# Optimization experiments

Measured on AMD Instinct MI355X. Metric: run time of the kernel, lower is better.

The kernel has to match this reference:

```python
import jax, jax.numpy as jnp
import numpy as np

N_DIS = 5000
N_GEN = 20000
N = N_DIS + N_GEN
E = 400000
N_MIRNA = 2000
EMB = 128
HID = 64


def setup_inputs() -> dict:
    key = jax.random.key(0)
    ks = jax.random.split(key, 20)
    def g(k, shape, scale=0.05):
        return jax.random.normal(k, shape, dtype=jnp.float32) * scale
    return {
        'd_features': g(ks[0], (N_DIS, 383), 1.0),
        'g_features': g(ks[1], (N_GEN, 4395), 1.0),
        'miRNA_dis': jax.random.uniform(ks[2], (N_MIRNA, N_DIS), dtype=jnp.float32),
        'gene_dis': jax.random.uniform(ks[3], (N_GEN, N_DIS), dtype=jnp.float32),
        'Wd': g(ks[4], (383, EMB)),
        'bd': jnp.zeros((EMB,), jnp.float32),
        'Wg': g(ks[5], (4395, EMB)),
        'bg': jnp.zeros((EMB,), jnp.float32),
        'W1': g(ks[6], (N_MIRNA, EMB)),
        'W4': g(ks[7], (N_DIS, EMB)),
        'Ws1': g(ks[8], (EMB, HID)),
        'Wn1': g(ks[9], (EMB, HID)),
        'b1': jnp.zeros((HID,), jnp.float32),
        'Ws2': g(ks[10], (HID, HID)),
        'Wn2': g(ks[11], (HID, HID)),
        'b2': jnp.zeros((HID,), jnp.float32),
        'src': jax.random.randint(ks[12], (E,), 0, N, dtype=jnp.int32),
        'dst': jax.random.randint(ks[13], (E,), 0, N, dtype=jnp.int32),
    }


def _sage_mean(h, src, dst, Ws, Wn, b):
    # DGL SAGEConv 'mean': fc_self(h) + fc_neigh(mean over in-neighbors) + bias
    msg = h[src]                                            # [E, d] gather
    agg = jax.ops.segment_sum(msg, dst, num_segments=N)     # [N, d] scatter-add
    deg = jax.ops.segment_sum(jnp.ones((dst.shape[0],), h.dtype), dst, num_segments=N)
    neigh = agg / jnp.maximum(deg, 1.0)[:, None]            # mean (zero-deg -> 0)
    return h @ Ws + neigh @ Wn + b


def reference(d_features, g_features, miRNA_dis, gene_dis, Wd, bd, Wg, bg,
              W1, W4, Ws1, Wn1, b1, Ws2, Wn2, b2, src, dst):
    # CrossCompressUnit outputs used by forward: A2 = M1^T W1, B1 = M2 W4
    A2 = miRNA_dis.T @ W1          # [N_DIS, EMB]
    B1 = gene_dis @ W4             # [N_GEN, EMB]
    # Node embeddings (dropout is identity at inference; torch.no_grad block)
    h_dis = 0.9 * (d_features @ Wd + bd) + 0.1 * A2   # [N_DIS, EMB]
    h_gen = 0.9 * (g_features @ Wg + bg) + 0.1 * B1   # [N_GEN, EMB]
    h = jnp.concatenate([h_dis, h_gen], axis=0)        # [N, EMB]
    h = _sage_mean(h, src, dst, Ws1, Wn1, b1)          # [N, 64]
    h = jax.nn.relu(h)
    h = _sage_mean(h, src, dst, Ws2, Wn2, b2)          # [N, 64]
    return h
```

## Files before the change

kernel.cpp:

```cpp
#include <hip/hip_runtime.h>

#define NDIS 5000
#define NGEN 20000
#define NTOT 25000
#define EDG  400000

typedef __attribute__((ext_vector_type(8))) short short8;
typedef __attribute__((ext_vector_type(4))) float f32x4;
typedef __attribute__((ext_vector_type(4), aligned(4))) float f32x4u;
typedef __attribute__((ext_vector_type(4))) unsigned int uint4v;
typedef __attribute__((ext_vector_type(2))) unsigned int uint2v;
typedef __attribute__((ext_vector_type(2), aligned(4))) unsigned int uint2a;

constexpr size_t AL(size_t x) { return (x + 255) & ~(size_t)255; }
constexpr size_t OFF_H0   = 0;
constexpr size_t OFF_PQ   = AL(OFF_H0  + (size_t)NTOT * 128 * 4);
constexpr size_t OFF_H1   = AL(OFF_PQ  + (size_t)NTOT * 128 * 4);
constexpr size_t OFF_DEG  = AL(OFF_H1  + (size_t)NTOT * 128 * 4);
constexpr size_t OFF_RS   = AL(OFF_DEG + (size_t)NTOT * 4);
constexpr size_t OFF_CUR  = AL(OFF_RS  + (size_t)(NTOT + 1) * 4);
constexpr size_t OFF_ESRC = AL(OFF_CUR + (size_t)NTOT * 4);
constexpr size_t OFF_MIT  = AL(OFF_ESRC + (size_t)EDG * 4);
constexpr size_t OFF_BDIS = AL(OFF_MIT + (size_t)5000 * 2048 * 2);
constexpr size_t OFF_BGEN = AL(OFF_BDIS + (size_t)8 * 76 * 512 * 2);
constexpr size_t OFF_BS1  = AL(OFF_BGEN + (size_t)8 * 300 * 512 * 2);
constexpr size_t OFF_BS2  = AL(OFF_BS1 + (size_t)8 * 4 * 512 * 2);

__device__ __forceinline__ ushort f2bf(float f) {
    unsigned u = __float_as_uint(f);
    u += 0x7fffu + ((u >> 16) & 1u);
    return (ushort)(u >> 16);
}

__device__ __forceinline__ unsigned cvtpk(float a, float b) {
    unsigned r;
    asm("v_cvt_pk_bf16_f32 %0, %1, %2" : "=v"(r) : "v"(a), "v"(b));
    return r;
}

__device__ __forceinline__ void MFMA(f32x4& d, short8 a, short8 b) {
    asm volatile("v_mfma_f32_16x16x32_bf16 %0, %1, %2, %0"
                 : "+v"(d) : "v"(a), "v"(b));
}

struct TcvtIns { const float* p[9]; };

__global__ __launch_bounds__(256) void k_tcvt_multi(TcvtIns ins, char* ws)
{
    constexpr int   TR[9]   = {383, 2000, 4395, 5000, 2000, 128, 128, 64, 64};
    constexpr int   TC[9]   = {128, 128, 128, 128, 5000, 64, 64, 64, 64};
    constexpr int   TKT[9]  = {76, 76, 300, 300, 2048 , 4, 4, 4, 4};
    constexpr int   TKO[9]  = {0, 12, 0, 140, 0, 0, 0, 0, 0};
    constexpr int   TRP[9]  = {384, 2048, 4480, 5120, 2048, 128, 128, 128, 128};
    constexpr int   TNOFF[9]= {0, 0, 0, 0, 0, 0, 64, 0, 64};
    constexpr int   TMODE[9]= {1, 1, 1, 1, 0, 1, 1, 1, 1};
    constexpr float TSC[9]  = {0.9f, 0.1f, 0.9f, 0.1f, 1.f, 1.f, 1.f, 1.f, 1.f};
    constexpr size_t TOUT[9]= {OFF_BDIS, OFF_BDIS, OFF_BGEN, OFF_BGEN, OFF_MIT,
                               OFF_BS1, OFF_BS1, OFF_BS2, OFF_BS2};
    constexpr int TNBX[9]   = {4, 4, 4, 4, 157, 2, 2, 2, 2};
    constexpr int PRE[10]   = {0, 48, 304, 864, 1504, 11552, 11560, 11568, 11576, 11584};

    int bid = blockIdx.x;
    int d = 0;
#pragma unroll
    for (int q = 1; q < 9; ++q) if (bid >= PRE[q]) d = q;
    int local = bid - PRE[d];
    int bx = local % TNBX[d], by = local / TNBX[d];
    const int R = TR[d], C = TC[d], KT = TKT[d], KO = TKO[d];
    const int Rp = TRP[d], noff = TNOFF[d];
    const float scale = TSC[d];
    const float* in = ins.p[d];
    ushort* out = (ushort*)(ws + TOUT[d]);

    __shared__ float t[32][33];
    int tx = threadIdx.x & 31, ty = threadIdx.x >> 5;
    int c0 = bx * 32, r0 = by * 32;
#pragma unroll
    for (int j = 0; j < 4; ++j) {
        int r = r0 + ty + j * 8, c = c0 + tx;
        t[ty + j * 8][tx] = (r < R && c < C) ? in[(size_t)r * C + c] : 0.f;
    }
    __syncthreads();
#pragma unroll
    for (int j = 0; j < 4; ++j) {
        int c = c0 + ty + j * 8, r = r0 + tx;
        if (c >= C || r >= Rp) continue;
        ushort bv = f2bf(scale * t[tx][ty + j * 8]);
        if (TMODE[d] == 0) {
            out[(size_t)c * KT + r] = bv;
        } else {
            int n = noff + c, k = r;
            out[(size_t)((n >> 4) * KT + KO + (k >> 5)) * 512 +
                ((k >> 3) & 3) * 128 + (n & 15) * 8 + (k & 7)] = bv;
        }
    }
}

template<int A2MODE, bool ATOMIC>
__global__ __launch_bounds__(256, 2) void gemm_st(
    const float* __restrict__ A1, int lda1, long lim1, int nst1,
    const void* __restrict__ A2v, int lda2, long lim2, int nst2,
    const ushort* __restrict__ Bf, int KT,
    float* __restrict__ C, int M, const float* __restrict__ bias)
{
    __shared__ ushort ldsH0[64 * 128];
    __shared__ ushort ldsL0[64 * 128];
    __shared__ ushort ldsH1[64 * 128];
    __shared__ ushort ldsL1[64 * 128];
    const int tid  = threadIdx.x;
    const int lane = tid & 63;
    const int w    = tid >> 6;
    const int fr = lane & 15, kq = lane >> 4;
    const int bm0 = blockIdx.x * 64;

    const int NSTT = nst1 + nst2;
    const int per = (NSTT + gridDim.y - 1) / gridDim.y;
    const int s0 = blockIdx.y * per;
    const int s1 = min(NSTT, s0 + per);
    const int NT = s1 - s0;
    if (NT <= 0) return;

    f32x4 acc[4][2];
#pragma unroll
    for (int i = 0; i < 4; ++i) { acc[i][0] = {0.f,0.f,0.f,0.f}; acc[i][1] = {0.f,0.f,0.f,0.f}; }

    uint4v faA[8], faB[8];
    short8 Breg0[4][2], Breg1[4][2];

    const int srow = w * 16 + (lane >> 5);
    const int scol = lane & 31;

    auto issueA = [&](int stg, uint4v* fa) {
        const bool r1 = (A2MODE == 0) || (stg < nst1);
#pragma unroll
        for (int i = 0; i < 8; ++i) {
            int r = bm0 + srow + i * 2;
            if (r1) {
                long e = (long)r * lda1 + (long)(stg << 7) + scol * 4;
                if (e > lim1 - 4) e = lim1 - 4;
                fa[i] = __builtin_bit_cast(uint4v, *(const f32x4u*)(A1 + e));
            } else if (A2MODE == 1) {
                long e = (long)r * lda2 + (long)((stg - nst1) << 7) + scol * 4;
                if (e > lim2 - 4) e = lim2 - 4;
                fa[i] = __builtin_bit_cast(uint4v, *(const f32x4u*)((const float*)A2v + e));
            } else {
                long e = (long)r * lda2 + (long)((stg - nst1) << 7) + scol * 4;
                if (e > lim2 - 4) e = lim2 - 4;
                uint2a v = *(const uint2a*)((const ushort*)A2v + e);
                fa[i][0] = v[0]; fa[i][1] = v[1];
            }
        }
    };
    auto issueB = [&](int stg, short8 (*BR)[2]) {
#pragma unroll
        for (int ks = 0; ks < 4; ++ks)
#pragma unroll
            for (int nf = 0; nf < 2; ++nf)
                BR[ks][nf] = *(const short8*)(
                    Bf + (size_t)((w * 2 + nf) * KT + stg * 4 + ks) * 512 + lane * 8);
    };
    auto writeT = [&](int stg, const uint4v* fa, ushort* bufH, ushort* bufL) {
        const bool cvt = (A2MODE != 2) || (stg < nst1);
        const int G = scol >> 1, h = lane & 1;
#pragma unroll
        for (int i = 0; i < 8; ++i) {
            int r = srow + i * 2;
            const size_t off = (size_t)r * 256 + ((G ^ (r & 7)) << 4) + h * 8;
            uint2v dh, dl;
            if (cvt) {
                f32x4 v = __builtin_bit_cast(f32x4, fa[i]);
                dh[0] = cvtpk(v[0], v[1]);
                dh[1] = cvtpk(v[2], v[3]);
                float h0f = __uint_as_float(dh[0] << 16);
                float h1f = __uint_as_float(dh[0] & 0xffff0000u);
                float h2f = __uint_as_float(dh[1] << 16);
                float h3f = __uint_as_float(dh[1] & 0xffff0000u);
                dl[0] = cvtpk(v[0] - h0f, v[1] - h1f);
                dl[1] = cvtpk(v[2] - h2f, v[3] - h3f);
            } else {
                dh[0] = fa[i][0]; dh[1] = fa[i][1];
                dl[0] = 0u; dl[1] = 0u;
            }
            *(uint2v*)((char*)bufH + off) = dh;
            *(uint2v*)((char*)bufL + off) = dl;
        }
    };

#define PHASE(T, BR, LDSH, LDSL, FAW, LWH, LWL)                              \
    {                                                                        \
        const int x7 = fr & 7;                                               \
        _Pragma("unroll")                                                    \
        for (int ks = 0; ks < 4; ++ks) {                                     \
            short8 af[4], al[4];                                             \
            _Pragma("unroll")                                                \
            for (int mf = 0; mf < 4; ++mf) {                                 \
                const int so = (((ks * 4 + kq) ^ x7) << 3);                  \
                af[mf] = *(const short8*)&LDSH[fr * 128 + mf * 2048 + so];   \
                al[mf] = *(const short8*)&LDSL[fr * 128 + mf * 2048 + so];   \
            }                                                                \
            _Pragma("unroll")                                                \
            for (int mf = 0; mf < 4; ++mf) {                                 \
                MFMA(acc[mf][0], af[mf], BR[ks][0]);                         \
                MFMA(acc[mf][1], af[mf], BR[ks][1]);                         \
                MFMA(acc[mf][0], al[mf], BR[ks][0]);                         \
                MFMA(acc[mf][1], al[mf], BR[ks][1]);                         \
            }                                                                \
        }                                                                    \
        if ((T) + 2 < NT) issueB(s0 + (T) + 2, BR);                          \
        __builtin_amdgcn_s_barrier();                                        \
        if ((T) + 1 < NT) {                                                  \
            writeT(s0 + (T) + 1, FAW, LWH, LWL);                             \
            if ((T) + 3 < NT) issueA(s0 + (T) + 3, FAW);                     \
            asm volatile("s_waitcnt lgkmcnt(0)" ::: "memory");               \
            __builtin_amdgcn_s_barrier();                                    \
        }                                                                    \
    }

    issueA(s0, faA); issueB(s0, Breg0);
    if (NT > 1) { issueA(s0 + 1, faB); issueB(s0 + 1, Breg1); }
    writeT(s0, faA, ldsH0, ldsL0);
    if (NT > 2) issueA(s0 + 2, faA);
    asm volatile("s_waitcnt lgkmcnt(0)" ::: "memory");
    __builtin_amdgcn_s_barrier();

    for (int t = 0; t < NT; t += 2) {
        PHASE(t, Breg0, ldsH0, ldsL0, faB, ldsH1, ldsL1);
        if (t + 1 < NT) PHASE(t + 1, Breg1, ldsH1, ldsL1, faA, ldsH0, ldsL0);
    }
#undef PHASE

    asm volatile("s_nop 7\n\ts_nop 7\n\ts_nop 7" ::: "memory");
#pragma unroll
    for (int mf = 0; mf < 4; ++mf)
#pragma unroll
        for (int nf = 0; nf < 2; ++nf)
#pragma unroll
            for (int r = 0; r < 4; ++r) {
                int row = bm0 + mf * 16 + kq * 4 + r;
                if (row < M) {
                    int col = w * 32 + nf * 16 + fr;
                    if (ATOMIC) {
                        atomicAdd(&C[(size_t)row * 128 + col], acc[mf][nf][r]);
                    } else {
                        float v = acc[mf][nf][r];
                        if (col < 64) v += bias[col];
                        C[(size_t)row * 128 + col] = v;
                    }
                }
            }
}

__global__ void k_binit(float* __restrict__ h0, const float* __restrict__ bd,
                        const float* __restrict__ bg) {
    int i = blockIdx.x * 256 + threadIdx.x;
    if (i >= NTOT * 128) return;
    int col = i & 127;
    h0[i] = 0.9f * ((i >> 7) < NDIS ? bd[col] : bg[col]);
}

__global__ void k_deg(const int* __restrict__ dst, int* __restrict__ deg, int E) {
    int e = blockIdx.x * blockDim.x + threadIdx.x;
    if (e < E) atomicAdd(&deg[dst[e]], 1);
}

__global__ __launch_bounds__(1024) void k_scan(const int* __restrict__ deg,
                                               int* __restrict__ row_start,
                                               int* __restrict__ cursor, int n) {
    __shared__ int wsum[16];
    __shared__ int carry_s;
    int t = threadIdx.x;
    int lane = t & 63, wid = t >> 6;
    if (t == 0) { carry_s = 0; row_start[0] = 0; }
    __syncthreads();
    for (int base = 0; base < n; base += 1024) {
        int i = base + t;
        int v = (i < n) ? deg[i] : 0;
        int x = v;
#pragma unroll
        for (int off = 1; off < 64; off <<= 1) {
            int y = __shfl_up(x, off, 64);
            if (lane >= off) x += y;
        }
        if (lane == 63) wsum[wid] = x;
        __syncthreads();
        if (wid == 0) {
            int s = (lane < 16) ? wsum[lane] : 0;
#pragma unroll
            for (int off = 1; off < 16; off <<= 1) {
                int y = __shfl_up(s, off, 64);
                if (lane >= off) s += y;
            }
            if (lane < 16) wsum[lane] = s;
        }
        __syncthreads();
        int pre = (wid > 0 ? wsum[wid - 1] : 0) + carry_s;
        int incl = x + pre;
        if (i < n) { row_start[i + 1] = incl; cursor[i] = incl - v; }
        __syncthreads();
        if (t == 1023) carry_s = incl;
        __syncthreads();
    }
}

__global__ void k_fill(const int* __restrict__ src, const int* __restrict__ dst,
                       int* __restrict__ cursor, int* __restrict__ esrc, int E) {
    int e = blockIdx.x * blockDim.x + threadIdx.x;
    if (e < E) {
        int pos = atomicAdd(&cursor[dst[e]], 1);
        esrc[pos] = src[e];
    }
}

__global__ __launch_bounds__(64) void k_agg(const float* __restrict__ PQ,
                                            const int* __restrict__ rs,
                                            const int* __restrict__ esrc,
                                            float* __restrict__ out, int ldout, int relu)
{
    int n = blockIdx.x, t = threadIdx.x;
    int s0 = rs[n], s1 = rs[n + 1];
    float a0 = 0.f, a1 = 0.f, a2 = 0.f, a3 = 0.f;
    int i = s0;
    for (; i + 4 <= s1; i += 4) {
        int e0 = esrc[i], e1 = esrc[i + 1], e2 = esrc[i + 2], e3 = esrc[i + 3];
        a0 += PQ[(size_t)e0 * 128 + 64 + t];
        a1 += PQ[(size_t)e1 * 128 + 64 + t];
        a2 += PQ[(size_t)e2 * 128 + 64 + t];
        a3 += PQ[(size_t)e3 * 128 + 64 + t];
    }
    for (; i < s1; ++i) a0 += PQ[(size_t)esrc[i] * 128 + 64 + t];
    float s = (a0 + a1) + (a2 + a3);
    float dg = (float)(s1 - s0);
    s /= fmaxf(dg, 1.f);
    float v = PQ[(size_t)n * 128 + t] + s;
    if (relu) v = fmaxf(v, 0.f);
    out[(size_t)n * ldout + t] = v;
}

extern "C" void kernel_launch(void* const* d_in, const int* in_sizes, int n_in,
                              void* d_out, int out_size, void* d_ws, size_t ws_size,
                              hipStream_t stream)
{
    const float* d_features = (const float*)d_in[0];
    const float* g_features = (const float*)d_in[1];
    const float* miRNA_dis  = (const float*)d_in[2];
    const float* gene_dis   = (const float*)d_in[3];
    const float* Wd  = (const float*)d_in[4];
    const float* bd  = (const float*)d_in[5];
    const float* Wg  = (const float*)d_in[6];
    const float* bg  = (const float*)d_in[7];
    const float* W1  = (const float*)d_in[8];
    const float* W4  = (const float*)d_in[9];
    const float* Ws1 = (const float*)d_in[10];
    const float* Wn1 = (const float*)d_in[11];
    const float* b1  = (const float*)d_in[12];
    const float* Ws2 = (const float*)d_in[13];
    const float* Wn2 = (const float*)d_in[14];
    const float* b2  = (const float*)d_in[15];
    const int* src = (const int*)d_in[16];
    const int* dst = (const int*)d_in[17];
    (void)in_sizes; (void)n_in; (void)out_size; (void)ws_size;

    char* ws = (char*)d_ws;
    float*  h0   = (float*)(ws + OFF_H0);
    float*  PQ   = (float*)(ws + OFF_PQ);
    float*  h1   = (float*)(ws + OFF_H1);
    int*    deg  = (int*)(ws + OFF_DEG);
    int*    rs   = (int*)(ws + OFF_RS);
    int*    cur  = (int*)(ws + OFF_CUR);
    int*    esrc = (int*)(ws + OFF_ESRC);
    ushort* miT  = (ushort*)(ws + OFF_MIT);
    ushort* Bdis = (ushort*)(ws + OFF_BDIS);
    ushort* Bgen = (ushort*)(ws + OFF_BGEN);
    ushort* Bs1  = (ushort*)(ws + OFF_BS1);
    ushort* Bs2  = (ushort*)(ws + OFF_BS2);

    hipMemsetAsync(deg, 0, (size_t)NTOT * 4, stream);
    hipMemsetAsync(h1, 0, (size_t)NTOT * 128 * 4, stream);
    k_deg<<<(EDG + 255) / 256, 256, 0, stream>>>(dst, deg, EDG);
    k_scan<<<1, 1024, 0, stream>>>(deg, rs, cur, NTOT);
    k_fill<<<(EDG + 255) / 256, 256, 0, stream>>>(src, dst, cur, esrc, EDG);

    TcvtIns ins;
    ins.p[0] = Wd;  ins.p[1] = W1;  ins.p[2] = Wg;  ins.p[3] = W4;
    ins.p[4] = miRNA_dis; ins.p[5] = Ws1; ins.p[6] = Wn1; ins.p[7] = Ws2; ins.p[8] = Wn2;
    k_tcvt_multi<<<11584, 256, 0, stream>>>(ins, ws);

    k_binit<<<(NTOT * 128 + 255) / 256, 256, 0, stream>>>(h0, bd, bg);
    gemm_st<2, true><<<dim3(79, 5), 256, 0, stream>>>(
        d_features, 383, (long)NDIS * 383, 3,
        miT, 2048, (long)NDIS * 2048, 16, Bdis, 76, h0, NDIS, nullptr);
    gemm_st<1, true><<<dim3(313, 4), 256, 0, stream>>>(
        g_features, 4395, (long)NGEN * 4395, 35,
        gene_dis, 5000, (long)NGEN * 5000, 40, Bgen, 300,
        h0 + (size_t)NDIS * 128, NGEN, nullptr);

    gemm_st<0, false><<<dim3(391, 1), 256, 0, stream>>>(
        h0, 128, (long)NTOT * 128, 1, nullptr, 0, 0, 0, Bs1, 4, PQ, NTOT, b1);
    k_agg<<<NTOT, 64, 0, stream>>>(PQ, rs, esrc, h1, 128, 1);

    gemm_st<0, false><<<dim3(391, 1), 256, 0, stream>>>(
        h1, 128, (long)NTOT * 128, 1, nullptr, 0, 0, 0, Bs2, 4, PQ, NTOT, b2);
    k_agg<<<NTOT, 64, 0, stream>>>(PQ, rs, esrc, (float*)d_out, 64, 0);
}
```

Before: 376.3 us.

## Split concatenated-K embedding GEMMs into separate per-operand launches with own split-K

```diff
diff --git a/kernel.cpp b/kernel.cpp
--- a/kernel.cpp
+++ b/kernel.cpp
@@ -21,9 +21,11 @@
 constexpr size_t OFF_CUR  = AL(OFF_RS  + (size_t)(NTOT + 1) * 4);
 constexpr size_t OFF_ESRC = AL(OFF_CUR + (size_t)NTOT * 4);
 constexpr size_t OFF_MIT  = AL(OFF_ESRC + (size_t)EDG * 4);
-constexpr size_t OFF_BDIS = AL(OFF_MIT + (size_t)5000 * 2048 * 2);
-constexpr size_t OFF_BGEN = AL(OFF_BDIS + (size_t)8 * 76 * 512 * 2);
-constexpr size_t OFF_BS1  = AL(OFF_BGEN + (size_t)8 * 300 * 512 * 2);
+constexpr size_t OFF_BWD  = AL(OFF_MIT + (size_t)5000 * 2048 * 2);
+constexpr size_t OFF_BW1  = AL(OFF_BWD + (size_t)8 * 12 * 512 * 2);
+constexpr size_t OFF_BWG  = AL(OFF_BW1 + (size_t)8 * 64 * 512 * 2);
+constexpr size_t OFF_BW4  = AL(OFF_BWG + (size_t)8 * 140 * 512 * 2);
+constexpr size_t OFF_BS1  = AL(OFF_BW4 + (size_t)8 * 160 * 512 * 2);
 constexpr size_t OFF_BS2  = AL(OFF_BS1 + (size_t)8 * 4 * 512 * 2);
 
 __device__ __forceinline__ ushort f2bf(float f) {
@@ -49,13 +51,12 @@
 {
     constexpr int   TR[9]   = {383, 2000, 4395, 5000, 2000, 128, 128, 64, 64};
     constexpr int   TC[9]   = {128, 128, 128, 128, 5000, 64, 64, 64, 64};
-    constexpr int   TKT[9]  = {76, 76, 300, 300, 2048 , 4, 4, 4, 4};
-    constexpr int   TKO[9]  = {0, 12, 0, 140, 0, 0, 0, 0, 0};
+    constexpr int   TKT[9]  = {12, 64, 140, 160, 2048 , 4, 4, 4, 4};
     constexpr int   TRP[9]  = {384, 2048, 4480, 5120, 2048, 128, 128, 128, 128};
     constexpr int   TNOFF[9]= {0, 0, 0, 0, 0, 0, 64, 0, 64};
     constexpr int   TMODE[9]= {1, 1, 1, 1, 0, 1, 1, 1, 1};
     constexpr float TSC[9]  = {0.9f, 0.1f, 0.9f, 0.1f, 1.f, 1.f, 1.f, 1.f, 1.f};
-    constexpr size_t TOUT[9]= {OFF_BDIS, OFF_BDIS, OFF_BGEN, OFF_BGEN, OFF_MIT,
+    constexpr size_t TOUT[9]= {OFF_BWD, OFF_BW1, OFF_BWG, OFF_BW4, OFF_MIT,
                                OFF_BS1, OFF_BS1, OFF_BS2, OFF_BS2};
     constexpr int TNBX[9]   = {4, 4, 4, 4, 157, 2, 2, 2, 2};
     constexpr int PRE[10]   = {0, 48, 304, 864, 1504, 11552, 11560, 11568, 11576, 11584};
@@ -66,7 +67,7 @@
     for (int q = 1; q < 9; ++q) if (bid >= PRE[q]) d = q;
     int local = bid - PRE[d];
     int bx = local % TNBX[d], by = local / TNBX[d];
-    const int R = TR[d], C = TC[d], KT = TKT[d], KO = TKO[d];
+    const int R = TR[d], C = TC[d], KT = TKT[d];
     const int Rp = TRP[d], noff = TNOFF[d];
     const float scale = TSC[d];
     const float* in = ins.p[d];
@@ -90,7 +91,7 @@
             out[(size_t)c * KT + r] = bv;
         } else {
             int n = noff + c, k = r;
-            out[(size_t)((n >> 4) * KT + KO + (k >> 5)) * 512 +
+            out[(size_t)((n >> 4) * KT + (k >> 5)) * 512 +
                 ((k >> 3) & 3) * 128 + (n & 15) * 8 + (k & 7)] = bv;
         }
     }
@@ -139,10 +140,6 @@
                 long e = (long)r * lda1 + (long)(stg << 7) + scol * 4;
                 if (e > lim1 - 4) e = lim1 - 4;
                 fa[i] = __builtin_bit_cast(uint4v, *(const f32x4u*)(A1 + e));
-            } else if (A2MODE == 1) {
-                long e = (long)r * lda2 + (long)((stg - nst1) << 7) + scol * 4;
-                if (e > lim2 - 4) e = lim2 - 4;
-                fa[i] = __builtin_bit_cast(uint4v, *(const f32x4u*)((const float*)A2v + e));
             } else {
                 long e = (long)r * lda2 + (long)((stg - nst1) << 7) + scol * 4;
                 if (e > lim2 - 4) e = lim2 - 4;
@@ -369,8 +366,10 @@
     int*    cur  = (int*)(ws + OFF_CUR);
     int*    esrc = (int*)(ws + OFF_ESRC);
     ushort* miT  = (ushort*)(ws + OFF_MIT);
-    ushort* Bdis = (ushort*)(ws + OFF_BDIS);
-    ushort* Bgen = (ushort*)(ws + OFF_BGEN);
+    ushort* Bwd  = (ushort*)(ws + OFF_BWD);
+    ushort* Bw1  = (ushort*)(ws + OFF_BW1);
+    ushort* Bwg  = (ushort*)(ws + OFF_BWG);
+    ushort* Bw4  = (ushort*)(ws + OFF_BW4);
     ushort* Bs1  = (ushort*)(ws + OFF_BS1);
     ushort* Bs2  = (ushort*)(ws + OFF_BS2);
 
@@ -386,13 +385,18 @@
     k_tcvt_multi<<<11584, 256, 0, stream>>>(ins, ws);
 
     k_binit<<<(NTOT * 128 + 255) / 256, 256, 0, stream>>>(h0, bd, bg);
-    gemm_st<2, true><<<dim3(79, 5), 256, 0, stream>>>(
+    gemm_st<0, true><<<dim3(79, 1), 256, 0, stream>>>(
         d_features, 383, (long)NDIS * 383, 3,
-        miT, 2048, (long)NDIS * 2048, 16, Bdis, 76, h0, NDIS, nullptr);
-    gemm_st<1, true><<<dim3(313, 4), 256, 0, stream>>>(
+        nullptr, 0, 0, 0, Bwd, 12, h0, NDIS, nullptr);
+    gemm_st<2, true><<<dim3(79, 3), 256, 0, stream>>>(
+        nullptr, 0, 0, 0,
+        miT, 2048, (long)NDIS * 2048, 16, Bw1, 64, h0, NDIS, nullptr);
+    gemm_st<0, true><<<dim3(313, 6), 256, 0, stream>>>(
         g_features, 4395, (long)NGEN * 4395, 35,
-        gene_dis, 5000, (long)NGEN * 5000, 40, Bgen, 300,
-        h0 + (size_t)NDIS * 128, NGEN, nullptr);
+        nullptr, 0, 0, 0, Bwg, 140, h0 + (size_t)NDIS * 128, NGEN, nullptr);
+    gemm_st<0, true><<<dim3(313, 7), 256, 0, stream>>>(
+        gene_dis, 5000, (long)NGEN * 5000, 40,
+        nullptr, 0, 0, 0, Bw4, 160, h0 + (size_t)NDIS * 128, NGEN, nullptr);
 
     gemm_st<0, false><<<dim3(391, 1), 256, 0, stream>>>(
         h0, 128, (long)NTOT * 128, 1, nullptr, 0, 0, 0, Bs1, 4, PQ, NTOT, b1);
```

Result: slower. 418.5 us (+11.2%).
